# Optimization experiments

Measured on AMD Instinct MI355X. Metric: run time of the kernel, lower is better.

## Reference

```python
import jax, jax.numpy as jnp
import numpy as np

DECAY = 0.99
EPS = 1e-05


def setup_inputs() -> dict:
    key = jax.random.key(0)
    k1, k2, k3, k4 = jax.random.split(key, 4)
    B, T, D, K = 16, 4096, 128, 1024
    return {
        "z": jax.random.normal(k1, (B, T, D), dtype=jnp.float32),
        "embedding": jax.random.normal(k2, (K, D), dtype=jnp.float32),
        "cluster_size": jax.random.uniform(k3, (K,), dtype=jnp.float32),
        "ema_w": jax.random.normal(k4, (K, D), dtype=jnp.float32),
    }


def reference(z, embedding, cluster_size, ema_w):
    B, T, D = z.shape
    K = embedding.shape[0]
    z_flat = z.reshape(B * T, D)

    # Squared-distance matrix [N, K]: ||z||^2 - 2 z E^T + ||E||^2
    dist = (
        jnp.sum(z_flat * z_flat, axis=1, keepdims=True)
        - 2.0 * (z_flat @ embedding.T)
        + jnp.sum(embedding * embedding, axis=1)
    )
    indices = jnp.argmin(dist, axis=1)  # [N]
    z_q = embedding[indices].reshape(B, T, D)

    # EMA codebook update (training branch); segment_sum == one_hot.T @ z, one_hot.sum(0)
    batch_cluster = jax.ops.segment_sum(
        jnp.ones((B * T,), dtype=z.dtype), indices, num_segments=K
    )
    new_cluster_size = cluster_size * DECAY + (1.0 - DECAY) * batch_cluster
    batch_ema = jax.ops.segment_sum(z_flat, indices, num_segments=K)
    new_ema_w = ema_w * DECAY + (1.0 - DECAY) * batch_ema

    n = jnp.sum(new_cluster_size)
    smoothed = (new_cluster_size + EPS) / (n + K * EPS) * n
    new_embedding = new_ema_w / smoothed[:, None]

    # Commitment loss on OLD codebook vectors (matches torch order of ops)
    loss_vq = jnp.mean(jnp.square(jax.lax.stop_gradient(z_q) - z))
    # Straight-through estimator
    z_q_st = z + jax.lax.stop_gradient(z_q - z)

    return (
        z_q_st,
        indices.reshape(B, T),
        loss_vq,
        new_embedding,
        new_cluster_size,
        new_ema_w,
    )
```

## Files before the change

kernel.cpp:

```cpp
#include <hip/hip_runtime.h>

#define K_CODES 1024
#define D_DIM 128
#define N_ROWS 65536
#define DECAY_F 0.99f
#define OMD_F 0.01f
#define EPS_F 1e-5f

#define EPAD 144
#define CHUNK_CODES 64
#define N_CHUNKS 16
#define CHUNK_USHORT (2 * CHUNK_CODES * EPAD)
#define NT 2
#define SEG_TILE 64

#define WS_CNT     0
#define WS_LOSS    1024
#define WS_BE      1028
#define WS_ZERO_END (1028 + 131072)
#define WS_ENORM   132100
#define WS_SMOOTH  133124
#define WS_CUR     134148
#define WS_FIDX    135172
#define WS_BUCKET  200708
#define WS_SCODE   266244
#define WS_EIMG    331780

typedef __bf16 bf8_t __attribute__((ext_vector_type(8)));
typedef float  f4_t  __attribute__((ext_vector_type(4)));

__device__ inline unsigned short f2bf_bits(float f) {
    __bf16 h = (__bf16)f;
    return __builtin_bit_cast(unsigned short, h);
}
__device__ inline float bf_bits2f(unsigned short u) {
    __bf16 h = __builtin_bit_cast(__bf16, u);
    return (float)h;
}

__device__ inline void gld16(const void* g, void* l) {
    __builtin_amdgcn_global_load_lds(
        (const __attribute__((address_space(1))) void*)g,
        (__attribute__((address_space(3))) void*)l, 16, 0, 0);
}

__global__ void vq_prep(const float* __restrict__ emb, float* __restrict__ enorm,
                        unsigned short* __restrict__ eimg) {
    int t = blockIdx.x * blockDim.x + threadIdx.x;
    int code = t >> 5;
    int q = t & 31;
    float4 v = ((const float4*)(emb + (size_t)code * D_DIM))[q];
    int chunk = code >> 6, c = code & 63;
    size_t hbase = (size_t)chunk * CHUNK_USHORT + (size_t)c * EPAD + q * 4;
    size_t lbase = hbase + (size_t)CHUNK_CODES * EPAD;
    float vv[4] = {v.x, v.y, v.z, v.w};
    ushort4 hi, lo;
    unsigned short* hp = (unsigned short*)&hi;
    unsigned short* lp = (unsigned short*)&lo;
#pragma unroll
    for (int i = 0; i < 4; ++i) {
        unsigned short hb = f2bf_bits(vv[i]);
        hp[i] = hb;
        lp[i] = f2bf_bits(vv[i] - bf_bits2f(hb));
    }
    *(ushort4*)(eimg + hbase) = hi;
    *(ushort4*)(eimg + lbase) = lo;

    float s = v.x * v.x + v.y * v.y + v.z * v.z + v.w * v.w;
#pragma unroll
    for (int o = 1; o < 32; o <<= 1) s += __shfl_xor(s, o, 64);
    if (q == 0) enorm[code] = s;
}

__device__ inline void top2_update(float s, int code, float& s1, int& i1, float& s2, int& i2) {
    bool b1 = s < s1;
    bool b2 = s < s2;
    s2 = b1 ? s1 : (b2 ? s : s2);
    i2 = b1 ? i1 : (b2 ? code : i2);
    s1 = b1 ? s : s1;
    i1 = b1 ? code : i1;
}

__device__ inline void top2_merge(float& s1, int& i1, float& s2, int& i2,
                                  float t1, int j1, float t2, int j2) {
    bool bf = (t1 < s1) || (t1 == s1 && j1 < i1);
    float ns1 = bf ? t1 : s1;  int ni1 = bf ? j1 : i1;
    float ca  = bf ? s1 : t1;  int ia  = bf ? i1 : j1;
    float cb  = bf ? t2 : s2;  int ib  = bf ? j2 : i2;
    bool bs = (ca < cb) || (ca == cb && ia < ib);
    s1 = ns1; i1 = ni1;
    s2 = bs ? ca : cb; i2 = bs ? ia : ib;
}

__global__ __launch_bounds__(256) void vq_score(
    const float* __restrict__ z, const unsigned short* __restrict__ eimg,
    const float* __restrict__ enorm_g, const float* __restrict__ emb,
    float* __restrict__ out_zq, float* __restrict__ out_idx,
    int* __restrict__ cnt, unsigned int* __restrict__ fidx,
    float* __restrict__ loss_acc)
{
    __shared__ __align__(16) unsigned short lds[2][CHUNK_USHORT];
    __shared__ __align__(16) float lds_en[K_CODES];

    const int tid  = threadIdx.x;
    const int wv   = tid >> 6;
    const int lane = tid & 63;
    const int l16  = lane & 15;
    const int quad = lane >> 4;
    const int rowbase = blockIdx.x * 128 + wv * 32;

    ((float4*)lds_en)[tid] = ((const float4*)enorm_g)[tid];

    {
        const char* gs = (const char*)eimg;
        char* ls = (char*)&lds[0][0];
        int wb = wv * 9216;
#pragma unroll
        for (int i = 0; i < 9; ++i)
            gld16(gs + wb + i * 1024 + lane * 16, ls + wb + i * 1024);
    }

    bf8_t zh[NT][4], zl[NT][4];
#pragma unroll
    for (int nt = 0; nt < NT; ++nt) {
        int row = rowbase + nt * 16 + l16;
        const float* zr = z + (size_t)row * D_DIM;
#pragma unroll
        for (int ks = 0; ks < 4; ++ks) {
            const float4* p = (const float4*)(zr + ks * 32 + quad * 8);
            float4 a = p[0], b = p[1];
            float v[8] = {a.x, a.y, a.z, a.w, b.x, b.y, b.z, b.w};
#pragma unroll
            for (int i = 0; i < 8; ++i) {
                __bf16 hh = (__bf16)v[i];
                zh[nt][ks][i] = hh;
                zl[nt][ks][i] = (__bf16)(v[i] - (float)hh);
            }
        }
    }

    float s1[NT], s2[NT];
    int   i1[NT], i2[NT];
#pragma unroll
    for (int nt = 0; nt < NT; ++nt) { s1[nt] = 3.4e38f; s2[nt] = 3.4e38f; i1[nt] = 0; i2[nt] = 0; }

    __syncthreads();

    for (int c = 0; c < N_CHUNKS; ++c) {
        const int cur = c & 1;
        if (c + 1 < N_CHUNKS) {
            const char* gs = (const char*)(eimg + (size_t)(c + 1) * CHUNK_USHORT);
            char* ls = (char*)&lds[1 - cur][0];
            int wb = wv * 9216;
#pragma unroll
            for (int i = 0; i < 9; ++i)
                gld16(gs + wb + i * 1024 + lane * 16, ls + wb + i * 1024);
        }
        const unsigned short* buf = &lds[cur][0];

#pragma unroll
        for (int cg = 0; cg < 2; ++cg) {
            f4_t acc[2][NT];
#pragma unroll
            for (int ct = 0; ct < 2; ++ct)
#pragma unroll
                for (int nt = 0; nt < NT; ++nt) acc[ct][nt] = (f4_t)(0.f);

#pragma unroll
            for (int ks = 0; ks < 4; ++ks) {
                bf8_t ah[2], al[2];
#pragma unroll
                for (int ct = 0; ct < 2; ++ct) {
                    int cl = cg * 32 + ct * 16 + l16;
                    int base = cl * EPAD + ks * 32 + quad * 8;
                    ah[ct] = *(const bf8_t*)&buf[base];
                    al[ct] = *(const bf8_t*)&buf[CHUNK_CODES * EPAD + base];
                }
#pragma unroll
                for (int ct = 0; ct < 2; ++ct)
#pragma unroll
                    for (int nt = 0; nt < NT; ++nt) {
                        acc[ct][nt] = __builtin_amdgcn_mfma_f32_16x16x32_bf16(
                            ah[ct], zh[nt][ks], acc[ct][nt], 0, 0, 0);
                        acc[ct][nt] = __builtin_amdgcn_mfma_f32_16x16x32_bf16(
                            al[ct], zh[nt][ks], acc[ct][nt], 0, 0, 0);
                        acc[ct][nt] = __builtin_amdgcn_mfma_f32_16x16x32_bf16(
                            ah[ct], zl[nt][ks], acc[ct][nt], 0, 0, 0);
                    }
            }

#pragma unroll
            for (int ct = 0; ct < 2; ++ct) {
                int cb = c * 64 + cg * 32 + ct * 16 + quad * 4;
                float4 en4 = *(const float4*)&lds_en[cb];
                float env[4] = {en4.x, en4.y, en4.z, en4.w};
#pragma unroll
                for (int nt = 0; nt < NT; ++nt)
#pragma unroll
                    for (int r = 0; r < 4; ++r) {
                        float s = env[r] - 2.0f * acc[ct][nt][r];
                        top2_update(s, cb + r, s1[nt], i1[nt], s2[nt], i2[nt]);
                    }
            }
        }
        __syncthreads();
    }

#pragma unroll
    for (int off = 16; off <= 32; off <<= 1) {
#pragma unroll
        for (int nt = 0; nt < NT; ++nt) {
            float t1 = __shfl_xor(s1[nt], off, 64);
            int   j1 = __shfl_xor(i1[nt], off, 64);
            float t2 = __shfl_xor(s2[nt], off, 64);
            int   j2 = __shfl_xor(i2[nt], off, 64);
            top2_merge(s1[nt], i1[nt], s2[nt], i2[nt], t1, j1, t2, j2);
        }
    }

    float ls = 0.f;
#pragma unroll
    for (int nt = 0; nt < NT; ++nt) {
        int row = rowbase + nt * 16 + l16;
        int j1 = i1[nt], j2 = i2[nt];

        const float4* zp  = (const float4*)(z   + (size_t)row * D_DIM);
        const float4* e1p = (const float4*)(emb + (size_t)j1  * D_DIM);
        const float4* e2p = (const float4*)(emb + (size_t)j2  * D_DIM);

        float4 zv[8], a1[8], a2[8];
#pragma unroll
        for (int ks = 0; ks < 4; ++ks) {
            int o = ks * 8 + quad * 2;
            zv[ks * 2]     = zp[o];   zv[ks * 2 + 1] = zp[o + 1];
            a1[ks * 2]     = e1p[o];  a1[ks * 2 + 1] = e1p[o + 1];
            a2[ks * 2]     = e2p[o];  a2[ks * 2 + 1] = e2p[o + 1];
        }
        float p1 = 0.f, p2 = 0.f;
#pragma unroll
        for (int i = 0; i < 8; ++i) {
            p1 += zv[i].x * a1[i].x + zv[i].y * a1[i].y + zv[i].z * a1[i].z + zv[i].w * a1[i].w;
            p2 += zv[i].x * a2[i].x + zv[i].y * a2[i].y + zv[i].z * a2[i].z + zv[i].w * a2[i].w;
        }
        p1 += __shfl_xor(p1, 16, 64); p1 += __shfl_xor(p1, 32, 64);
        p2 += __shfl_xor(p2, 16, 64); p2 += __shfl_xor(p2, 32, 64);
        float sc1 = lds_en[j1] - 2.0f * p1;
        float sc2 = lds_en[j2] - 2.0f * p2;
        bool use2 = (sc2 < sc1) || (sc2 == sc1 && j2 < j1);
        int best = use2 ? j2 : j1;

        if (quad == 0) {
            out_idx[row] = (float)best;
            fidx[row] = (unsigned int)best;
            atomicAdd(cnt + best, 1);
        }

        float4* oz = (float4*)(out_zq + (size_t)row * D_DIM);
#pragma unroll
        for (int i = 0; i < 8; ++i) {
            float4 q = use2 ? a2[i] : a1[i];
            float4 zvv = zv[i];
            float4 df = {q.x - zvv.x, q.y - zvv.y, q.z - zvv.z, q.w - zvv.w};
            ls += df.x * df.x + df.y * df.y + df.z * df.z + df.w * df.w;
            float4 o = {zvv.x + df.x, zvv.y + df.y, zvv.z + df.z, zvv.w + df.w};
            oz[(i >> 1) * 8 + quad * 2 + (i & 1)] = o;
        }
    }

#pragma unroll
    for (int off = 32; off > 0; off >>= 1) ls += __shfl_down(ls, off, 64);
    if (lane == 0) atomicAdd(loss_acc, ls);
}

__global__ void vq_scan(const int* __restrict__ cnt, int* __restrict__ cursor)
{
    __shared__ int tmp[K_CODES];
    int k = threadIdx.x;
    int c = cnt[k];
    tmp[k] = c;
    __syncthreads();
    for (int off = 1; off < K_CODES; off <<= 1) {
        int t = (k >= off) ? tmp[k - off] : 0;
        __syncthreads();
        tmp[k] += t;
        __syncthreads();
    }
    cursor[k] = tmp[k] - c;
}

__global__ void vq_scatter(const unsigned int* __restrict__ fidx,
                           int* __restrict__ cursor, unsigned int* __restrict__ bucket,
                           int* __restrict__ scode)
{
    int row = blockIdx.x * blockDim.x + threadIdx.x;
    int k = (int)fidx[row];
    int slot = atomicAdd(cursor + k, 1);
    bucket[slot] = (unsigned int)row;
    scode[slot]  = k;
}

__global__ __launch_bounds__(128) void vq_segsum(
    const float* __restrict__ z, const unsigned int* __restrict__ bucket,
    const int* __restrict__ scode, float* __restrict__ be)
{
    __shared__ int sb[SEG_TILE];
    __shared__ int sc[SEG_TILE];
    const int tid = threadIdx.x;
    const int t0  = blockIdx.x * SEG_TILE;

    if (tid < SEG_TILE) sb[tid] = (int)bucket[t0 + tid];
    else if (tid < 2 * SEG_TILE) sc[tid - SEG_TILE] = scode[t0 + tid - SEG_TILE];
    __syncthreads();

    const int d = tid;
    float acc = 0.f;
    int cur = sc[0];

    for (int i = 0; i < SEG_TILE; i += 8) {
        float v[8];
#pragma unroll
        for (int j = 0; j < 8; ++j)
            v[j] = z[(size_t)sb[i + j] * D_DIM + d];
#pragma unroll
        for (int j = 0; j < 8; ++j) {
            int c = sc[i + j];
            if (c != cur) {
                atomicAdd(be + (size_t)cur * D_DIM + d, acc);
                acc = 0.f;
                cur = c;
            }
            acc += v[j];
        }
    }
    atomicAdd(be + (size_t)cur * D_DIM + d, acc);
}

__global__ void vq_finalize1(const float* __restrict__ cs, const int* __restrict__ cnt,
                             const float* __restrict__ loss_acc,
                             float* __restrict__ out_ncs, float* __restrict__ out_loss,
                             float* __restrict__ smoothed)
{
    __shared__ float red[K_CODES];
    int k = threadIdx.x;
    float ncs = cs[k] * DECAY_F + OMD_F * (float)cnt[k];
    out_ncs[k] = ncs;
    red[k] = ncs;
    __syncthreads();
    for (int s = 512; s > 0; s >>= 1) {
        if (k < s) red[k] += red[k + s];
        __syncthreads();
    }
    float n = red[0];
    smoothed[k] = (ncs + EPS_F) / (n + (float)K_CODES * EPS_F) * n;
    if (k == 0) out_loss[0] = loss_acc[0] / (float)((size_t)N_ROWS * D_DIM);
}

__global__ void vq_finalize2(const float* __restrict__ ema_w, const float* __restrict__ be,
                             const float* __restrict__ smoothed,
                             float* __restrict__ out_emb, float* __restrict__ out_ema)
{
    int i = blockIdx.x * blockDim.x + threadIdx.x;
    float e = ema_w[i] * DECAY_F + OMD_F * be[i];
    out_ema[i] = e;
    out_emb[i] = e / smoothed[i >> 7];
}

extern "C" void kernel_launch(void* const* d_in, const int* in_sizes, int n_in,
                              void* d_out, int out_size, void* d_ws, size_t ws_size,
                              hipStream_t stream) {
    const float* z   = (const float*)d_in[0];
    const float* emb = (const float*)d_in[1];
    const float* cs  = (const float*)d_in[2];
    const float* ema = (const float*)d_in[3];

    float* out    = (float*)d_out;
    float* o_zq   = out;
    float* o_idx  = o_zq + (size_t)N_ROWS * D_DIM;
    float* o_loss = o_idx + N_ROWS;
    float* o_emb  = o_loss + 1;
    float* o_ncs  = o_emb + K_CODES * D_DIM;
    float* o_ema  = o_ncs + K_CODES;

    float* ws = (float*)d_ws;
    int*            cnt      = (int*)(ws + WS_CNT);
    float*          lacc     = ws + WS_LOSS;
    float*          be       = ws + WS_BE;
    float*          enorm    = ws + WS_ENORM;
    float*          smoothed = ws + WS_SMOOTH;
    int*            cursor   = (int*)(ws + WS_CUR);
    unsigned int*   fidx     = (unsigned int*)(ws + WS_FIDX);
    unsigned int*   bucket   = (unsigned int*)(ws + WS_BUCKET);
    int*            scode    = (int*)(ws + WS_SCODE);
    unsigned short* eimg     = (unsigned short*)(ws + WS_EIMG);

    hipMemsetAsync(ws, 0, (size_t)WS_ZERO_END * sizeof(float), stream);
    vq_prep<<<128, 256, 0, stream>>>(emb, enorm, eimg);
    vq_score<<<512, 256, 0, stream>>>(z, eimg, enorm, emb,
                                      o_zq, o_idx, cnt, fidx, lacc);
    vq_scan<<<1, K_CODES, 0, stream>>>(cnt, cursor);
    vq_scatter<<<N_ROWS / 256, 256, 0, stream>>>(fidx, cursor, bucket, scode);
    vq_segsum<<<N_ROWS / SEG_TILE, 128, 0, stream>>>(z, bucket, scode, be);
    vq_finalize1<<<1, K_CODES, 0, stream>>>(cs, cnt, lacc, o_ncs, o_loss, smoothed);
    vq_finalize2<<<K_CODES * D_DIM / 256, 256, 0, stream>>>(ema, be, smoothed, o_emb, o_ema);
}
```

Before: 213.5 us.

## Triple-buffer codebook chunks with explicit vmcnt waits and one barrier per chunk

Halves the codebook chunk to 32 codes and moves the main scoring loop from a double-buffered LDS ring to a triple-buffered one. Loads are issued two chunks ahead, with s_waitcnt vmcnt(5) and a single scheduling-fenced barrier per iteration in place of the trailing __syncthreads. The aim is to hide global-to-LDS latency more deeply and cut barrier stalls. In exchange there are twice as many loop iterations and barriers, a different LDS padding (EPAD 160), and a reliance on hand-counted vmcnt that must match the number of outstanding loads per wave.

```diff
diff --git a/kernel.cpp b/kernel.cpp
--- a/kernel.cpp
+++ b/kernel.cpp
@@ -7,12 +7,14 @@
 #define OMD_F 0.01f
 #define EPS_F 1e-5f
 
-#define EPAD 144
-#define CHUNK_CODES 64
-#define N_CHUNKS 16
+#define EPAD 160
+#define CHUNK_CODES 32
+#define N_CHUNKS 32
 #define CHUNK_USHORT (2 * CHUNK_CODES * EPAD)
+#define NBUF 3
 #define NT 2
 #define SEG_TILE 64
+#define LPW 5
 
 #define WS_CNT     0
 #define WS_LOSS    1024
@@ -44,13 +46,20 @@
         (__attribute__((address_space(3))) void*)l, 16, 0, 0);
 }
 
+#define WAITVM5() asm volatile("s_waitcnt vmcnt(5)" ::: "memory")
+#define WAITVM0() asm volatile("s_waitcnt vmcnt(0)" ::: "memory")
+#define LGKM0()   asm volatile("s_waitcnt lgkmcnt(0)" ::: "memory")
+#define SBAR() do { __builtin_amdgcn_sched_barrier(0); \
+                    __builtin_amdgcn_s_barrier(); \
+                    __builtin_amdgcn_sched_barrier(0); } while (0)
+
 __global__ void vq_prep(const float* __restrict__ emb, float* __restrict__ enorm,
                         unsigned short* __restrict__ eimg) {
     int t = blockIdx.x * blockDim.x + threadIdx.x;
     int code = t >> 5;
     int q = t & 31;
     float4 v = ((const float4*)(emb + (size_t)code * D_DIM))[q];
-    int chunk = code >> 6, c = code & 63;
+    int chunk = code >> 5, c = code & 31;
     size_t hbase = (size_t)chunk * CHUNK_USHORT + (size_t)c * EPAD + q * 4;
     size_t lbase = hbase + (size_t)CHUNK_CODES * EPAD;
     float vv[4] = {v.x, v.y, v.z, v.w};
@@ -99,7 +108,7 @@
     int* __restrict__ cnt, unsigned int* __restrict__ fidx,
     float* __restrict__ loss_acc)
 {
-    __shared__ __align__(16) unsigned short lds[2][CHUNK_USHORT];
+    __shared__ __align__(16) unsigned short lds[NBUF * CHUNK_USHORT];
     __shared__ __align__(16) float lds_en[K_CODES];
 
     const int tid  = threadIdx.x;
@@ -111,15 +120,6 @@
 
     ((float4*)lds_en)[tid] = ((const float4*)enorm_g)[tid];
 
-    {
-        const char* gs = (const char*)eimg;
-        char* ls = (char*)&lds[0][0];
-        int wb = wv * 9216;
-#pragma unroll
-        for (int i = 0; i < 9; ++i)
-            gld16(gs + wb + i * 1024 + lane * 16, ls + wb + i * 1024);
-    }
-
     bf8_t zh[NT][4], zl[NT][4];
 #pragma unroll
     for (int nt = 0; nt < NT; ++nt) {
@@ -139,71 +139,134 @@
         }
     }
 
+    {
+        const char* gs = (const char*)eimg;
+#pragma unroll
+        for (int i = 0; i < LPW; ++i) {
+            int idx = wv * LPW + i;
+            gld16(gs + idx * 1024 + lane * 16, (char*)lds + idx * 1024);
+        }
+        gs += CHUNK_USHORT * 2;
+#pragma unroll
+        for (int i = 0; i < LPW; ++i) {
+            int idx = wv * LPW + i;
+            gld16(gs + idx * 1024 + lane * 16, (char*)lds + CHUNK_USHORT * 2 + idx * 1024);
+        }
+    }
+
     float s1[NT], s2[NT];
     int   i1[NT], i2[NT];
 #pragma unroll
     for (int nt = 0; nt < NT; ++nt) { s1[nt] = 3.4e38f; s2[nt] = 3.4e38f; i1[nt] = 0; i2[nt] = 0; }
 
-    __syncthreads();
-
-    for (int c = 0; c < N_CHUNKS; ++c) {
-        const int cur = c & 1;
-        if (c + 1 < N_CHUNKS) {
-            const char* gs = (const char*)(eimg + (size_t)(c + 1) * CHUNK_USHORT);
-            char* ls = (char*)&lds[1 - cur][0];
-            int wb = wv * 9216;
-#pragma unroll
-            for (int i = 0; i < 9; ++i)
-                gld16(gs + wb + i * 1024 + lane * 16, ls + wb + i * 1024);
-        }
-        const unsigned short* buf = &lds[cur][0];
-
-#pragma unroll
-        for (int cg = 0; cg < 2; ++cg) {
-            f4_t acc[2][NT];
+    LGKM0();
+
+    for (int c = 0; c < N_CHUNKS - 1; ++c) {
+        WAITVM5();
+        SBAR();
+        if (c + 2 < N_CHUNKS) {
+            const char* gs = (const char*)eimg + (size_t)(c + 2) * CHUNK_USHORT * 2;
+            char* ls = (char*)lds + ((c + 2) % NBUF) * CHUNK_USHORT * 2;
+#pragma unroll
+            for (int i = 0; i < LPW; ++i) {
+                int idx = wv * LPW + i;
+                gld16(gs + idx * 1024 + lane * 16, ls + idx * 1024);
+            }
+        }
+        const unsigned short* buf = &lds[(c % NBUF) * CHUNK_USHORT];
+
+        f4_t acc[2][NT];
+#pragma unroll
+        for (int ct = 0; ct < 2; ++ct)
+#pragma unroll
+            for (int nt = 0; nt < NT; ++nt) acc[ct][nt] = (f4_t)(0.f);
+
+#pragma unroll
+        for (int ks = 0; ks < 4; ++ks) {
+            bf8_t ah[2], al[2];
+#pragma unroll
+            for (int ct = 0; ct < 2; ++ct) {
+                int cl = ct * 16 + l16;
+                int base = cl * EPAD + ks * 32 + quad * 8;
+                ah[ct] = *(const bf8_t*)&buf[base];
+                al[ct] = *(const bf8_t*)&buf[CHUNK_CODES * EPAD + base];
+            }
 #pragma unroll
             for (int ct = 0; ct < 2; ++ct)
 #pragma unroll
-                for (int nt = 0; nt < NT; ++nt) acc[ct][nt] = (f4_t)(0.f);
-
-#pragma unroll
-            for (int ks = 0; ks < 4; ++ks) {
-                bf8_t ah[2], al[2];
-#pragma unroll
-                for (int ct = 0; ct < 2; ++ct) {
-                    int cl = cg * 32 + ct * 16 + l16;
-                    int base = cl * EPAD + ks * 32 + quad * 8;
-                    ah[ct] = *(const bf8_t*)&buf[base];
-                    al[ct] = *(const bf8_t*)&buf[CHUNK_CODES * EPAD + base];
+                for (int nt = 0; nt < NT; ++nt) {
+                    acc[ct][nt] = __builtin_amdgcn_mfma_f32_16x16x32_bf16(
+                        ah[ct], zh[nt][ks], acc[ct][nt], 0, 0, 0);
+                    acc[ct][nt] = __builtin_amdgcn_mfma_f32_16x16x32_bf16(
+                        al[ct], zh[nt][ks], acc[ct][nt], 0, 0, 0);
+                    acc[ct][nt] = __builtin_amdgcn_mfma_f32_16x16x32_bf16(
+                        ah[ct], zl[nt][ks], acc[ct][nt], 0, 0, 0);
                 }
-#pragma unroll
-                for (int ct = 0; ct < 2; ++ct)
-#pragma unroll
-                    for (int nt = 0; nt < NT; ++nt) {
-                        acc[ct][nt] = __builtin_amdgcn_mfma_f32_16x16x32_bf16(
-                            ah[ct], zh[nt][ks], acc[ct][nt], 0, 0, 0);
-                        acc[ct][nt] = __builtin_amdgcn_mfma_f32_16x16x32_bf16(
-                            al[ct], zh[nt][ks], acc[ct][nt], 0, 0, 0);
-                        acc[ct][nt] = __builtin_amdgcn_mfma_f32_16x16x32_bf16(
-                            ah[ct], zl[nt][ks], acc[ct][nt], 0, 0, 0);
-                    }
+        }
+
+#pragma unroll
+        for (int ct = 0; ct < 2; ++ct) {
+            int cb = c * 32 + ct * 16 + quad * 4;
+            float4 en4 = *(const float4*)&lds_en[cb];
+            float env[4] = {en4.x, en4.y, en4.z, en4.w};
+#pragma unroll
+            for (int nt = 0; nt < NT; ++nt)
+#pragma unroll
+                for (int r = 0; r < 4; ++r) {
+                    float s = env[r] - 2.0f * acc[ct][nt][r];
+                    top2_update(s, cb + r, s1[nt], i1[nt], s2[nt], i2[nt]);
+                }
+        }
+    }
+
+    {
+        const int c = N_CHUNKS - 1;
+        WAITVM0();
+        SBAR();
+        const unsigned short* buf = &lds[(c % NBUF) * CHUNK_USHORT];
+
+        f4_t acc[2][NT];
+#pragma unroll
+        for (int ct = 0; ct < 2; ++ct)
+#pragma unroll
+            for (int nt = 0; nt < NT; ++nt) acc[ct][nt] = (f4_t)(0.f);
+
+#pragma unroll
+        for (int ks = 0; ks < 4; ++ks) {
+            bf8_t ah[2], al[2];
+#pragma unroll
+            for (int ct = 0; ct < 2; ++ct) {
+                int cl = ct * 16 + l16;
+                int base = cl * EPAD + ks * 32 + quad * 8;
+                ah[ct] = *(const bf8_t*)&buf[base];
+                al[ct] = *(const bf8_t*)&buf[CHUNK_CODES * EPAD + base];
             }
-
-#pragma unroll
-            for (int ct = 0; ct < 2; ++ct) {
-                int cb = c * 64 + cg * 32 + ct * 16 + quad * 4;
-                float4 en4 = *(const float4*)&lds_en[cb];
-                float env[4] = {en4.x, en4.y, en4.z, en4.w};
-#pragma unroll
-                for (int nt = 0; nt < NT; ++nt)
-#pragma unroll
-                    for (int r = 0; r < 4; ++r) {
-                        float s = env[r] - 2.0f * acc[ct][nt][r];
-                        top2_update(s, cb + r, s1[nt], i1[nt], s2[nt], i2[nt]);
-                    }
-            }
-        }
-        __syncthreads();
+#pragma unroll
+            for (int ct = 0; ct < 2; ++ct)
+#pragma unroll
+                for (int nt = 0; nt < NT; ++nt) {
+                    acc[ct][nt] = __builtin_amdgcn_mfma_f32_16x16x32_bf16(
+                        ah[ct], zh[nt][ks], acc[ct][nt], 0, 0, 0);
+                    acc[ct][nt] = __builtin_amdgcn_mfma_f32_16x16x32_bf16(
+                        al[ct], zh[nt][ks], acc[ct][nt], 0, 0, 0);
+                    acc[ct][nt] = __builtin_amdgcn_mfma_f32_16x16x32_bf16(
+                        ah[ct], zl[nt][ks], acc[ct][nt], 0, 0, 0);
+                }
+        }
+
+#pragma unroll
+        for (int ct = 0; ct < 2; ++ct) {
+            int cb = c * 32 + ct * 16 + quad * 4;
+            float4 en4 = *(const float4*)&lds_en[cb];
+            float env[4] = {en4.x, en4.y, en4.z, en4.w};
+#pragma unroll
+            for (int nt = 0; nt < NT; ++nt)
+#pragma unroll
+                for (int r = 0; r < 4; ++r) {
+                    float s = env[r] - 2.0f * acc[ct][nt][r];
+                    top2_update(s, cb + r, s1[nt], i1[nt], s2[nt], i2[nt]);
+                }
+        }
     }
 
 #pragma unroll
```

After: 229.6 us. 7.5% more time.

## Fold workspace zeroing into prep, merge finalize into scan, pack bucket entries

Applied to the files above, without the earlier changes.

Removes the hipMemsetAsync by zeroing the counter, loss and batch-EMA workspace inside vq_prep. Merges vq_finalize1 into vq_scan and rewrites the scan with wave shuffles instead of a barrier-heavy shared-memory loop. Packs row and code into one 64-bit entry so the scatter writes one word, and doubles the segsum tile to 128 rows. Together these cut launch count and small-kernel latency, at the cost of larger segsum tiles giving fewer blocks.

```diff
diff --git a/kernel.cpp b/kernel.cpp
--- a/kernel.cpp
+++ b/kernel.cpp
@@ -12,7 +12,7 @@
 #define N_CHUNKS 16
 #define CHUNK_USHORT (2 * CHUNK_CODES * EPAD)
 #define NT 2
-#define SEG_TILE 64
+#define SEG_TILE 128
 
 #define WS_CNT     0
 #define WS_LOSS    1024
@@ -23,7 +23,6 @@
 #define WS_CUR     134148
 #define WS_FIDX    135172
 #define WS_BUCKET  200708
-#define WS_SCODE   266244
 #define WS_EIMG    331780
 
 typedef __bf16 bf8_t __attribute__((ext_vector_type(8)));
@@ -45,8 +44,13 @@
 }
 
 __global__ void vq_prep(const float* __restrict__ emb, float* __restrict__ enorm,
-                        unsigned short* __restrict__ eimg) {
+                        unsigned short* __restrict__ eimg,
+                        float4* __restrict__ zero_head, float4* __restrict__ zero_be) {
     int t = blockIdx.x * blockDim.x + threadIdx.x;
+    float4 z4 = {0.f, 0.f, 0.f, 0.f};
+    if (t < 257) zero_head[t] = z4;
+    zero_be[t] = z4;
+
     int code = t >> 5;
     int q = t & 31;
     float4 v = ((const float4*)(emb + (size_t)code * D_DIM))[q];
@@ -272,44 +276,68 @@
     if (lane == 0) atomicAdd(loss_acc, ls);
 }
 
-__global__ void vq_scan(const int* __restrict__ cnt, int* __restrict__ cursor)
+__global__ void vq_scan(const int* __restrict__ cnt, int* __restrict__ cursor,
+                        const float* __restrict__ cs, const float* __restrict__ lacc,
+                        float* __restrict__ out_ncs, float* __restrict__ out_loss,
+                        float* __restrict__ smoothed)
 {
-    __shared__ int tmp[K_CODES];
+    __shared__ int   wsum[16];
+    __shared__ float fr[16];
     int k = threadIdx.x;
+    int wv = k >> 6, lane = k & 63;
     int c = cnt[k];
-    tmp[k] = c;
+
+    int x = c;
+#pragma unroll
+    for (int off = 1; off < 64; off <<= 1) {
+        int t = __shfl_up(x, off, 64);
+        if (lane >= off) x += t;
+    }
+    if (lane == 63) wsum[wv] = x;
+
+    float ncs = cs[k] * DECAY_F + OMD_F * (float)c;
+    out_ncs[k] = ncs;
+    float s = ncs;
+#pragma unroll
+    for (int o = 1; o < 64; o <<= 1) s += __shfl_xor(s, o, 64);
+    if (lane == 0) fr[wv] = s;
     __syncthreads();
-    for (int off = 1; off < K_CODES; off <<= 1) {
-        int t = (k >= off) ? tmp[k - off] : 0;
-        __syncthreads();
-        tmp[k] += t;
-        __syncthreads();
-    }
-    cursor[k] = tmp[k] - c;
+
+    int woff = 0; float n = 0.f;
+#pragma unroll
+    for (int i = 0; i < 16; ++i) {
+        if (i < wv) woff += wsum[i];
+        n += fr[i];
+    }
+    cursor[k] = woff + x - c;
+    smoothed[k] = (ncs + EPS_F) / (n + (float)K_CODES * EPS_F) * n;
+    if (k == 0) out_loss[0] = lacc[0] / (float)((size_t)N_ROWS * D_DIM);
 }
 
 __global__ void vq_scatter(const unsigned int* __restrict__ fidx,
-                           int* __restrict__ cursor, unsigned int* __restrict__ bucket,
-                           int* __restrict__ scode)
+                           int* __restrict__ cursor,
+                           unsigned long long* __restrict__ packed)
 {
     int row = blockIdx.x * blockDim.x + threadIdx.x;
     int k = (int)fidx[row];
     int slot = atomicAdd(cursor + k, 1);
-    bucket[slot] = (unsigned int)row;
-    scode[slot]  = k;
+    packed[slot] = ((unsigned long long)(unsigned)k << 32) | (unsigned)row;
 }
 
 __global__ __launch_bounds__(128) void vq_segsum(
-    const float* __restrict__ z, const unsigned int* __restrict__ bucket,
-    const int* __restrict__ scode, float* __restrict__ be)
+    const float* __restrict__ z, const unsigned long long* __restrict__ packed,
+    float* __restrict__ be)
 {
     __shared__ int sb[SEG_TILE];
     __shared__ int sc[SEG_TILE];
     const int tid = threadIdx.x;
     const int t0  = blockIdx.x * SEG_TILE;
 
-    if (tid < SEG_TILE) sb[tid] = (int)bucket[t0 + tid];
-    else if (tid < 2 * SEG_TILE) sc[tid - SEG_TILE] = scode[t0 + tid - SEG_TILE];
+    {
+        unsigned long long v = packed[t0 + tid];
+        sb[tid] = (int)(unsigned)(v & 0xffffffffu);
+        sc[tid] = (int)(v >> 32);
+    }
     __syncthreads();
 
     const int d = tid;
@@ -335,26 +363,6 @@
     atomicAdd(be + (size_t)cur * D_DIM + d, acc);
 }
 
-__global__ void vq_finalize1(const float* __restrict__ cs, const int* __restrict__ cnt,
-                             const float* __restrict__ loss_acc,
-                             float* __restrict__ out_ncs, float* __restrict__ out_loss,
-                             float* __restrict__ smoothed)
-{
-    __shared__ float red[K_CODES];
-    int k = threadIdx.x;
-    float ncs = cs[k] * DECAY_F + OMD_F * (float)cnt[k];
-    out_ncs[k] = ncs;
-    red[k] = ncs;
-    __syncthreads();
-    for (int s = 512; s > 0; s >>= 1) {
-        if (k < s) red[k] += red[k + s];
-        __syncthreads();
-    }
-    float n = red[0];
-    smoothed[k] = (ncs + EPS_F) / (n + (float)K_CODES * EPS_F) * n;
-    if (k == 0) out_loss[0] = loss_acc[0] / (float)((size_t)N_ROWS * D_DIM);
-}
-
 __global__ void vq_finalize2(const float* __restrict__ ema_w, const float* __restrict__ be,
                              const float* __restrict__ smoothed,
                              float* __restrict__ out_emb, float* __restrict__ out_ema)
@@ -382,24 +390,22 @@
     float* o_ema  = o_ncs + K_CODES;
 
     float* ws = (float*)d_ws;
-    int*            cnt      = (int*)(ws + WS_CNT);
-    float*          lacc     = ws + WS_LOSS;
-    float*          be       = ws + WS_BE;
-    float*          enorm    = ws + WS_ENORM;
-    float*          smoothed = ws + WS_SMOOTH;
-    int*            cursor   = (int*)(ws + WS_CUR);
-    unsigned int*   fidx     = (unsigned int*)(ws + WS_FIDX);
-    unsigned int*   bucket   = (unsigned int*)(ws + WS_BUCKET);
-    int*            scode    = (int*)(ws + WS_SCODE);
-    unsigned short* eimg     = (unsigned short*)(ws + WS_EIMG);
-
-    hipMemsetAsync(ws, 0, (size_t)WS_ZERO_END * sizeof(float), stream);
-    vq_prep<<<128, 256, 0, stream>>>(emb, enorm, eimg);
+    int*                 cnt      = (int*)(ws + WS_CNT);
+    float*               lacc     = ws + WS_LOSS;
+    float*               be       = ws + WS_BE;
+    float*               enorm    = ws + WS_ENORM;
+    float*               smoothed = ws + WS_SMOOTH;
+    int*                 cursor   = (int*)(ws + WS_CUR);
+    unsigned int*        fidx     = (unsigned int*)(ws + WS_FIDX);
+    unsigned long long*  packed   = (unsigned long long*)(ws + WS_BUCKET);
+    unsigned short*      eimg     = (unsigned short*)(ws + WS_EIMG);
+
+    vq_prep<<<128, 256, 0, stream>>>(emb, enorm, eimg,
+                                     (float4*)(ws + WS_CNT), (float4*)(ws + WS_BE));
     vq_score<<<512, 256, 0, stream>>>(z, eimg, enorm, emb,
                                       o_zq, o_idx, cnt, fidx, lacc);
-    vq_scan<<<1, K_CODES, 0, stream>>>(cnt, cursor);
-    vq_scatter<<<N_ROWS / 256, 256, 0, stream>>>(fidx, cursor, bucket, scode);
-    vq_segsum<<<N_ROWS / SEG_TILE, 128, 0, stream>>>(z, bucket, scode, be);
-    vq_finalize1<<<1, K_CODES, 0, stream>>>(cs, cnt, lacc, o_ncs, o_loss, smoothed);
+    vq_scan<<<1, K_CODES, 0, stream>>>(cnt, cursor, cs, lacc, o_ncs, o_loss, smoothed);
+    vq_scatter<<<N_ROWS / 256, 256, 0, stream>>>(fidx, cursor, packed);
+    vq_segsum<<<N_ROWS / SEG_TILE, 128, 0, stream>>>(z, packed, be);
     vq_finalize2<<<K_CODES * D_DIM / 256, 256, 0, stream>>>(ema, be, smoothed, o_emb, o_ema);
 }
```

Result: no change. 214.2 us (median of 2 runs) (+0.3%).
